# Kernel tuning notes

Measured on AMD Instinct MI355X. Metric: run time of the kernel, lower is better.

Reference implementation:

```python
import jax, jax.numpy as jnp
import numpy as np

PATCH = 7
STACK = 16
TUBE = 2
IMG = 84
EMBED = 1024
GH = IMG // PATCH   # 12
GW = IMG // PATCH   # 12
GD = STACK // TUBE  # 8
PF = 1 * PATCH * PATCH  # per-frame patch feature (C*p*p) = 49


def _sincos_1d(dim, pos):
    # pos: [N] -> [N, dim]
    omega = 1.0 / (10000.0 ** (np.arange(dim // 2, dtype=np.float64) / (dim / 2.0)))
    out = pos[:, None].astype(np.float64) * omega[None, :]
    return np.concatenate([np.sin(out), np.cos(out)], axis=1)


def get_3d_sincos_pos_embed(grid_h, grid_w, grid_depth, embed_dim):
    # standard video sincos split: 1/4 temporal, 3/4 spatial (half h, half w)
    dim_t = embed_dim // 4
    dim_s = embed_dim - dim_t
    emb_t = _sincos_1d(dim_t, np.arange(grid_depth))            # [D, dim_t]
    emb_h = _sincos_1d(dim_s // 2, np.arange(grid_h))           # [gh, dim_s/2]
    emb_w = _sincos_1d(dim_s - dim_s // 2, np.arange(grid_w))   # [gw, ...]
    # spatial tokens row-major (h major, w minor), matching unfold ordering
    emb_hw = np.concatenate(
        [np.repeat(emb_h, grid_w, axis=0), np.tile(emb_w, (grid_h, 1))], axis=1
    )  # [gh*gw, dim_s]
    ns = grid_h * grid_w
    # token order: depth major, spatial minor (matches D*Ns reshape in forward)
    pe = np.concatenate(
        [np.repeat(emb_t, ns, axis=0), np.tile(emb_hw, (grid_depth, 1))], axis=1
    )  # [D*Ns, embed_dim]
    return pe.astype(np.float32)


def setup_inputs() -> dict:
    key = jax.random.key(0)
    k1, k2, k3 = jax.random.split(key, 3)
    B = 64
    video = jax.random.normal(k1, (B, STACK, 1, IMG, IMG), dtype=jnp.float32)
    tubelet_in = TUBE * PF  # 98
    W = jax.random.normal(k2, (EMBED, tubelet_in), dtype=jnp.float32) * (tubelet_in ** -0.5)
    b = jax.random.normal(k3, (EMBED,), dtype=jnp.float32) * 0.02
    pos_embed = jnp.asarray(get_3d_sincos_pos_embed(GH, GW, GD, EMBED))[None]  # [1, N, E]
    return {"video": video, "W": W, "b": b, "pos_embed": pos_embed}


def reference(video, W, b, pos_embed):
    B, T, C, H, W_ = video.shape
    p = PATCH
    gh, gw = H // p, W_ // p
    ns = gh * gw
    # extract_tensor_patches (stride == window, no padding): pure reshape/transpose
    x = video.reshape(B * T, C, gh, p, gw, p)
    x = x.transpose(0, 2, 4, 1, 3, 5)                 # [BT, gh, gw, C, p, p]
    x = x.reshape(B, T, ns, C * p * p)                # [B, T, Ns, Pf]
    x = x.reshape(B, GD, TUBE, ns, C * p * p)
    x = x.transpose(0, 1, 3, 2, 4)                    # [B, D, Ns, Ts, Pf]
    tubelets = x.reshape(B, GD * ns, TUBE * C * p * p)  # [B, N, 98]
    tokens = jnp.einsum("bnk,ek->bne", tubelets, W) + b + pos_embed
    return tokens
```

## Files before the change

### kernel.cpp

```cpp
#include <hip/hip_runtime.h>
#include <hip/hip_bf16.h>
#include <stdint.h>


typedef __bf16 bf16_t;
typedef bf16_t bf16x8 __attribute__((ext_vector_type(8)));
typedef float f32x4 __attribute__((ext_vector_type(4)));

#define B_      64
#define N_TOK   1152
#define M_TOT   (B_ * N_TOK)
#define E_      1024
#define KP      128
#define K_REAL  98
#define BM      128
#define BN      128
#define MT_N    (M_TOT / BM)
#define NT_N    (E_ / BN)

__global__ void wconv_kernel(const float* __restrict__ W, bf16_t* __restrict__ Wb) {
    int idx = blockIdx.x * 256 + threadIdx.x;
    int k = idx & (KP - 1);
    int e = idx >> 7;
    float v = (k < K_REAL) ? W[e * K_REAL + k] : 0.f;
    Wb[idx] = (bf16_t)v;
}

__global__ void im2col_kernel(const float* __restrict__ video, bf16_t* __restrict__ A) {
    int idx = blockIdx.x * 256 + threadIdx.x;
    int k = idx & (KP - 1);
    int m = idx >> 7;
    float v = 0.f;
    if (k < K_REAL) {
        int b  = m / N_TOK;
        int n  = m - b * N_TOK;
        int d  = n / 144, s = n - d * 144;
        int ts = (k >= 49) ? 1 : 0;
        int f  = k - ts * 49;
        int i  = s / 12, j = s - i * 12;
        int fy = f / 7,  fx = f - fy * 7;
        int t  = d * 2 + ts;
        int y  = i * 7 + fy;
        int x  = j * 7 + fx;
        v = video[(b * 16 + t) * 7056 + y * 84 + x];
    }
    A[idx] = (bf16_t)v;
}

__global__ __launch_bounds__(256) void gemm_kernel(
    const bf16_t* __restrict__ A, const bf16_t* __restrict__ Wb,
    const float* __restrict__ bias, const float* __restrict__ pos,
    float* __restrict__ out) {
    __shared__ __align__(16) bf16_t As[BM * KP];
    __shared__ __align__(16) bf16_t Bs[BN * KP];

    const int tid  = threadIdx.x;
    const int wv   = tid >> 6;
    const int lane = tid & 63;

    const int bid = blockIdx.x;
    const int mt  = bid % MT_N;
    const int nt  = bid / MT_N;
    const long m0 = (long)mt * BM;
    const int  n0 = nt * BN;

    {
        const char* gA = (const char*)(A + m0 * KP);
        const char* gB = (const char*)(Wb + (long)n0 * KP);
        char* lA = (char*)As;
        char* lB = (char*)Bs;
#pragma unroll
        for (int i = 0; i < 8; ++i) {
            int off = (wv * 8 + i) * 1024;
            __builtin_amdgcn_global_load_lds(
                (const __attribute__((address_space(1))) void*)(gA + off + lane * 16),
                (__attribute__((address_space(3))) void*)(lA + off), 16, 0, 0);
        }
#pragma unroll
        for (int i = 0; i < 8; ++i) {
            int off = (wv * 8 + i) * 1024;
            __builtin_amdgcn_global_load_lds(
                (const __attribute__((address_space(1))) void*)(gB + off + lane * 16),
                (__attribute__((address_space(3))) void*)(lB + off), 16, 0, 0);
        }
    }
    __syncthreads();

    const int wr = wv >> 1, wc = wv & 1;
    const int lr = lane & 15;
    const int lk = (lane >> 4) * 8;

    f32x4 acc[4][4];
#pragma unroll
    for (int mi = 0; mi < 4; ++mi)
#pragma unroll
        for (int ni = 0; ni < 4; ++ni)
            acc[mi][ni] = (f32x4){0.f, 0.f, 0.f, 0.f};

#pragma unroll
    for (int kk = 0; kk < 4; ++kk) {
        bf16x8 a[4], b[4];
#pragma unroll
        for (int mi = 0; mi < 4; ++mi)
            a[mi] = *(const bf16x8*)&As[(wr * 64 + mi * 16 + lr) * KP + kk * 32 + lk];
#pragma unroll
        for (int ni = 0; ni < 4; ++ni)
            b[ni] = *(const bf16x8*)&Bs[(wc * 64 + ni * 16 + lr) * KP + kk * 32 + lk];
#pragma unroll
        for (int mi = 0; mi < 4; ++mi)
#pragma unroll
            for (int ni = 0; ni < 4; ++ni)
                acc[mi][ni] = __builtin_amdgcn_mfma_f32_16x16x32_bf16(
                    a[mi], b[ni], acc[mi][ni], 0, 0, 0);
    }

    const int ntok_blk = (mt % 9) * BM;
    const int row4 = (lane >> 4) * 4;
#pragma unroll
    for (int ni = 0; ni < 4; ++ni) {
        const int e  = n0 + wc * 64 + ni * 16 + lr;
        const float be = bias[e];
#pragma unroll
        for (int mi = 0; mi < 4; ++mi) {
            const int mloc = wr * 64 + mi * 16 + row4;
            const long mg  = m0 + mloc;
            const int ntok = ntok_blk + mloc;
#pragma unroll
            for (int r = 0; r < 4; ++r) {
                out[(mg + r) * (long)E_ + e] =
                    acc[mi][ni][r] + be + pos[(ntok + r) * E_ + e];
            }
        }
    }
}

extern "C" void kernel_launch(void* const* d_in, const int* in_sizes, int n_in,
                              void* d_out, int out_size, void* d_ws, size_t ws_size,
                              hipStream_t stream) {
    const float* video = (const float*)d_in[0];
    const float* W     = (const float*)d_in[1];
    const float* bias  = (const float*)d_in[2];
    const float* pos   = (const float*)d_in[3];
    float* out = (float*)d_out;

    bf16_t* A_ws = (bf16_t*)d_ws;
    bf16_t* W_ws = (bf16_t*)((char*)d_ws + (size_t)M_TOT * KP * 2);

    wconv_kernel<<<(E_ * KP) / 256, 256, 0, stream>>>(W, W_ws);
    im2col_kernel<<<(M_TOT * KP) / 256, 256, 0, stream>>>(video, A_ws);
    gemm_kernel<<<MT_N * NT_N, 256, 0, stream>>>(A_ws, W_ws, bias, pos, out);
}
```

Before: 455.8 us.

## Swizzle LDS layout via pre-swizzled im2col/W, vectorize im2col, nontemporal output stores

Measured after the change: 443.9 us. 2.6% less time.

```diff
diff --git a/kernel.cpp b/kernel.cpp
--- a/kernel.cpp
+++ b/kernel.cpp
@@ -23,28 +23,33 @@
     int k = idx & (KP - 1);
     int e = idx >> 7;
     float v = (k < K_REAL) ? W[e * K_REAL + k] : 0.f;
-    Wb[idx] = (bf16_t)v;
+    Wb[e * KP + (k ^ ((e & 7) << 3))] = (bf16_t)v;
 }
 
 __global__ void im2col_kernel(const float* __restrict__ video, bf16_t* __restrict__ A) {
     int idx = blockIdx.x * 256 + threadIdx.x;
-    int k = idx & (KP - 1);
-    int m = idx >> 7;
-    float v = 0.f;
-    if (k < K_REAL) {
-        int b  = m / N_TOK;
-        int n  = m - b * N_TOK;
-        int d  = n / 144, s = n - d * 144;
-        int ts = (k >= 49) ? 1 : 0;
-        int f  = k - ts * 49;
-        int i  = s / 12, j = s - i * 12;
-        int fy = f / 7,  fx = f - fy * 7;
-        int t  = d * 2 + ts;
-        int y  = i * 7 + fy;
-        int x  = j * 7 + fx;
-        v = video[(b * 16 + t) * 7056 + y * 84 + x];
+    int g = idx & 15;
+    int m = idx >> 4;
+    int b  = m / N_TOK;
+    int n  = m - b * N_TOK;
+    int d  = n / 144, s = n - d * 144;
+    int i  = s / 12,  jj = s - i * 12;
+    const float* base = video + (b * 16 + d * 2) * 7056 + (i * 7) * 84 + jj * 7;
+    bf16_t vals[8];
+#pragma unroll
+    for (int j = 0; j < 8; ++j) {
+        int k = g * 8 + j;
+        float v = 0.f;
+        if (k < K_REAL) {
+            int ts = (k >= 49) ? 1 : 0;
+            int f  = k - ts * 49;
+            int fy = f / 7, fx = f - fy * 7;
+            v = base[ts * 7056 + fy * 84 + fx];
+        }
+        vals[j] = (bf16_t)v;
     }
-    A[idx] = (bf16_t)v;
+    int col = (g * 8) ^ ((m & 7) << 3);
+    *(bf16x8*)&A[(long)m * KP + col] = *(const bf16x8*)vals;
 }
 
 __global__ __launch_bounds__(256) void gemm_kernel(
@@ -89,6 +94,7 @@
     const int wr = wv >> 1, wc = wv & 1;
     const int lr = lane & 15;
     const int lk = (lane >> 4) * 8;
+    const int xsw = (lr & 7) << 3;
 
     f32x4 acc[4][4];
 #pragma unroll
@@ -100,12 +106,13 @@
 #pragma unroll
     for (int kk = 0; kk < 4; ++kk) {
         bf16x8 a[4], b[4];
+        const int col = (kk * 32 + lk) ^ xsw;
 #pragma unroll
         for (int mi = 0; mi < 4; ++mi)
-            a[mi] = *(const bf16x8*)&As[(wr * 64 + mi * 16 + lr) * KP + kk * 32 + lk];
+            a[mi] = *(const bf16x8*)&As[(wr * 64 + mi * 16 + lr) * KP + col];
 #pragma unroll
         for (int ni = 0; ni < 4; ++ni)
-            b[ni] = *(const bf16x8*)&Bs[(wc * 64 + ni * 16 + lr) * KP + kk * 32 + lk];
+            b[ni] = *(const bf16x8*)&Bs[(wc * 64 + ni * 16 + lr) * KP + col];
 #pragma unroll
         for (int mi = 0; mi < 4; ++mi)
 #pragma unroll
@@ -127,8 +134,8 @@
             const int ntok = ntok_blk + mloc;
 #pragma unroll
             for (int r = 0; r < 4; ++r) {
-                out[(mg + r) * (long)E_ + e] =
-                    acc[mi][ni][r] + be + pos[(ntok + r) * E_ + e];
+                float vout = acc[mi][ni][r] + be + pos[(ntok + r) * E_ + e];
+                __builtin_nontemporal_store(vout, &out[(mg + r) * (long)E_ + e]);
             }
         }
     }
@@ -147,6 +154,6 @@
     bf16_t* W_ws = (bf16_t*)((char*)d_ws + (size_t)M_TOT * KP * 2);
 
     wconv_kernel<<<(E_ * KP) / 256, 256, 0, stream>>>(W, W_ws);
-    im2col_kernel<<<(M_TOT * KP) / 256, 256, 0, stream>>>(video, A_ws);
+    im2col_kernel<<<(M_TOT * 16) / 256, 256, 0, stream>>>(video, A_ws);
     gemm_kernel<<<MT_N * NT_N, 256, 0, stream>>>(A_ws, W_ws, bias, pos, out);
 }
```
